# Performance work log

Hardware: AMD Instinct MI355X
Metric: run time of the kernel (lower is better)

## Reference

```python
import jax, jax.numpy as jnp
import numpy as np

EMBED_DIM = 1024
NUM_HEADS = 16
HEAD_DIM = EMBED_DIM // NUM_HEADS


def setup_inputs() -> dict:
    key = jax.random.key(0)
    ks = jax.random.split(key, 6)
    s = 1.0 / np.sqrt(EMBED_DIM)
    x = jax.random.normal(ks[0], (2, 2048, EMBED_DIM), dtype=jnp.float32)
    Wk = jax.random.uniform(ks[1], (EMBED_DIM, EMBED_DIM), jnp.float32, -s, s)
    Wq = jax.random.uniform(ks[2], (EMBED_DIM, EMBED_DIM), jnp.float32, -s, s)
    Wv = jax.random.uniform(ks[3], (EMBED_DIM, EMBED_DIM), jnp.float32, -s, s)
    Wo = jax.random.uniform(ks[4], (EMBED_DIM, EMBED_DIM), jnp.float32, -s, s)
    bo = jax.random.uniform(ks[5], (EMBED_DIM,), jnp.float32, -s, s)
    return {"x": x, "Wq": Wq, "Wk": Wk, "Wv": Wv, "Wo": Wo, "bo": bo}


def reference(x, Wq, Wk, Wv, Wo, bo):
    b, s, e = x.shape
    h, d = NUM_HEADS, HEAD_DIM
    scale = d ** (-0.5)
    # nn.Linear: y = x @ W.T ; here W stored as [out, in] -> use W.T
    q = (x @ Wq.T).reshape(b, s, h, d).transpose(0, 2, 1, 3)  # b h s d
    k = (x @ Wk.T).reshape(b, s, h, d).transpose(0, 2, 1, 3)
    v = (x @ Wv.T).reshape(b, s, h, d).transpose(0, 2, 1, 3)
    logits = jnp.einsum('bhqd,bhkd->bhqk', q, k) * scale
    attn = jax.nn.softmax(logits, axis=-1)
    out = jnp.einsum('bhqk,bhkd->bhqd', attn, v)
    out = out.transpose(0, 2, 1, 3).reshape(b, s, e)
    return out @ Wo.T + bo
```

## Files before the change

### kernel.cpp

```cpp
#include <hip/hip_runtime.h>
#include <hip/hip_bf16.h>

using short8 = __attribute__((ext_vector_type(8))) short;
using f32x4  = __attribute__((ext_vector_type(4))) float;
using uint4v = __attribute__((ext_vector_type(4))) unsigned;

#if __has_builtin(__builtin_amdgcn_exp2f)
#define EXP2(x) __builtin_amdgcn_exp2f(x)
#else
#define EXP2(x) exp2f(x)
#endif

#define SOFT_BARRIER()                                            \
    do {                                                          \
        asm volatile("s_waitcnt lgkmcnt(0)" ::: "memory");        \
        __builtin_amdgcn_s_barrier();                             \
    } while (0)

__device__ __forceinline__ short f2bf(float f) {
    union { float f; unsigned u; } v; v.f = f;
    unsigned r = v.u + 0x7fffu + ((v.u >> 16) & 1u);
    return (short)(r >> 16);
}
__device__ __forceinline__ unsigned pack_trunc(float a, float b) {
    union { float f; unsigned u; } ua, ub; ua.f = a; ub.f = b;
#if __has_builtin(__builtin_amdgcn_perm)
    return __builtin_amdgcn_perm(ub.u, ua.u, 0x07060302u);
#else
    return (ub.u & 0xFFFF0000u) | (ua.u >> 16);
#endif
}
__device__ __forceinline__ void async_copy16(const short* g, short* s) {
    __builtin_amdgcn_global_load_lds(
        (const __attribute__((address_space(1))) void*)g,
        (__attribute__((address_space(3))) void*)s, 16, 0, 0);
}

__global__ __launch_bounds__(256) void cvt_f32_bf16(
    const float* __restrict__ s0, const float* __restrict__ s1,
    const float* __restrict__ s2, const float* __restrict__ s3,
    const float* __restrict__ s4,
    short* __restrict__ d0, short* __restrict__ d1, short* __restrict__ d2,
    short* __restrict__ d3, short* __restrict__ d4) {
    const int bid = blockIdx.x;
    const float* s; short* d; int base;
    if (bid < 4096) {
        s = s0; d = d0; base = bid << 10;
    } else {
        const int r = bid - 4096;
        base = (r & 1023) << 10;
        switch (r >> 10) {
            case 0: s = s1; d = d1; break;
            case 1: s = s2; d = d2; break;
            case 2: s = s3; d = d3; break;
            default: s = s4; d = d4; break;
        }
    }
    const int idx = base + threadIdx.x * 4;
    float4 v = *(const float4*)(s + idx);
    short4 o;
    o.x = f2bf(v.x); o.y = f2bf(v.y); o.z = f2bf(v.z); o.w = f2bf(v.w);
    *(short4*)(d + idx) = o;
}

template <int MODE>
__device__ __forceinline__ void gemm_body(const short* __restrict__ A,
                                          const short* __restrict__ B,
                                          short* __restrict__ C,
                                          float scale,
                                          short* __restrict__ As,
                                          short* __restrict__ Bs,
                                          int bm, int bn) {
    constexpr int Kd = 1024, Nd = 1024, Sd = 2048;

    const int tid  = threadIdx.x;
    const int w    = tid >> 6, lane = tid & 63;
    const int quad = lane >> 4, l16 = lane & 15;
    const int xr   = l16 & 7;
    const int wm   = (w >> 1) * 64, wn = (w & 1) * 64;

    f32x4 acc[4][4];
#pragma unroll
    for (int i = 0; i < 4; ++i)
#pragma unroll
        for (int j = 0; j < 4; ++j) acc[i][j] = (f32x4){0.f, 0.f, 0.f, 0.f};

    for (int k0 = 0; k0 < Kd; k0 += 64) {
        __syncthreads();
#pragma unroll
        for (int c = 0; c < 4; ++c) {
            int li   = c * 256 + tid;
            int row  = li >> 3;
            int gcol = ((li & 7) ^ (row & 7)) * 8;
            async_copy16(A + (size_t)(bm + row) * Kd + k0 + gcol, &As[li * 8]);
            async_copy16(B + (size_t)(bn + row) * Kd + k0 + gcol, &Bs[li * 8]);
        }
        __syncthreads();

#pragma unroll
        for (int kk = 0; kk < 2; ++kk) {
            short8 af[4], bfv[4];
#pragma unroll
            for (int mi = 0; mi < 4; ++mi) {
                const int r = wm + mi * 16 + l16;
                af[mi] = *(const short8*)(
                    &As[r * 64 + (((kk * 4 + quad) ^ xr) * 8)]);
            }
#pragma unroll
            for (int ni = 0; ni < 4; ++ni) {
                const int r = wn + ni * 16 + l16;
                bfv[ni] = *(const short8*)(
                    &Bs[r * 64 + (((kk * 4 + quad) ^ xr) * 8)]);
            }
#pragma unroll
            for (int mi = 0; mi < 4; ++mi)
#pragma unroll
                for (int ni = 0; ni < 4; ++ni) {
                    if constexpr (MODE == 2)
                        acc[mi][ni] = __builtin_amdgcn_mfma_f32_16x16x32_bf16(
                            bfv[ni], af[mi], acc[mi][ni], 0, 0, 0);
                    else
                        acc[mi][ni] = __builtin_amdgcn_mfma_f32_16x16x32_bf16(
                            af[mi], bfv[ni], acc[mi][ni], 0, 0, 0);
                }
        }
    }

    if constexpr (MODE == 2) {
#pragma unroll
        for (int mi = 0; mi < 4; ++mi) {
            const int m_g = bm + wm + mi * 16 + l16;
            const int b_  = m_g >> 11, s_ = m_g & 2047;
#pragma unroll
            for (int ni = 0; ni < 4; ++ni)
#pragma unroll
                for (int r = 0; r < 4; ++r) {
                    const int n_g = bn + wn + ni * 16 + quad * 4 + r;
                    C[(size_t)b_ * Nd * Sd + (size_t)n_g * Sd + s_] =
                        f2bf(acc[mi][ni][r]);
                }
        }
    } else {
#pragma unroll
        for (int ni = 0; ni < 4; ++ni) {
            const int colg = bn + wn + ni * 16 + l16;
#pragma unroll
            for (int mi = 0; mi < 4; ++mi)
#pragma unroll
                for (int r = 0; r < 4; ++r) {
                    const int rowg = bm + wm + mi * 16 + quad * 4 + r;
                    C[(size_t)rowg * Nd + colg] = f2bf(acc[mi][ni][r] * scale);
                }
        }
    }
}

#define CSC 0.18033688f

__global__ __launch_bounds__(256, 3) void proj_gemm(
    const short* __restrict__ X,
    const short* __restrict__ Wq, const short* __restrict__ Wk,
    const short* __restrict__ Wv,
    short* __restrict__ Qo, short* __restrict__ Ko, short* __restrict__ VTo) {
    __shared__ __align__(16) short As[128 * 64];
    __shared__ __align__(16) short Bs[128 * 64];

    const int bid = blockIdx.x;
    const int xcd = bid & 7, idx = bid >> 3;
    const int z   = idx >> 5;
    const int rem = idx & 31;
    const int bm  = (((xcd >> 1) * 8) + (rem >> 2)) * 128;
    const int bn  = (((xcd & 1) * 4) + (rem & 3)) * 128;

    if (z == 0)
        gemm_body<0>(X, Wq, Qo, CSC, As, Bs, bm, bn);
    else if (z == 1)
        gemm_body<0>(X, Wk, Ko, 1.0f, As, Bs, bm, bn);
    else
        gemm_body<2>(X, Wv, VTo, 1.0f, As, Bs, bm, bn);
}

__global__ __launch_bounds__(256, 2) void out_gemm(
    const short* __restrict__ A, const short* __restrict__ B,
    const float* __restrict__ bias, float* __restrict__ C) {
    constexpr int Kd = 1024, Nd = 1024;
    __shared__ __align__(16) short As[64 * 64];
    __shared__ __align__(16) short Bs[128 * 64];

    const int tid  = threadIdx.x;
    const int w    = tid >> 6, lane = tid & 63;
    const int quad = lane >> 4, l16 = lane & 15;
    const int xr   = l16 & 7;
    const int wm   = (w >> 1) * 32, wn = (w & 1) * 64;

    const int bid = blockIdx.x;
    const int xcd = bid & 7, idx = bid >> 3;
    const int bm  = (((xcd >> 1) * 16) + (idx >> 2)) * 64;
    const int bn  = (((xcd & 1) * 4) + (idx & 3)) * 128;

    f32x4 acc[2][4];
#pragma unroll
    for (int i = 0; i < 2; ++i)
#pragma unroll
        for (int j = 0; j < 4; ++j) acc[i][j] = (f32x4){0.f, 0.f, 0.f, 0.f};

    for (int k0 = 0; k0 < Kd; k0 += 64) {
        __syncthreads();
#pragma unroll
        for (int c = 0; c < 2; ++c) {
            int li   = c * 256 + tid;
            int row  = li >> 3;
            int gcol = ((li & 7) ^ (row & 7)) * 8;
            async_copy16(A + (size_t)(bm + row) * Kd + k0 + gcol, &As[li * 8]);
        }
#pragma unroll
        for (int c = 0; c < 4; ++c) {
            int li   = c * 256 + tid;
            int row  = li >> 3;
            int gcol = ((li & 7) ^ (row & 7)) * 8;
            async_copy16(B + (size_t)(bn + row) * Kd + k0 + gcol, &Bs[li * 8]);
        }
        __syncthreads();

#pragma unroll
        for (int kk = 0; kk < 2; ++kk) {
            short8 af[2], bfv[4];
#pragma unroll
            for (int mi = 0; mi < 2; ++mi) {
                const int r = wm + mi * 16 + l16;
                af[mi] = *(const short8*)(
                    &As[r * 64 + (((kk * 4 + quad) ^ xr) * 8)]);
            }
#pragma unroll
            for (int ni = 0; ni < 4; ++ni) {
                const int r = wn + ni * 16 + l16;
                bfv[ni] = *(const short8*)(
                    &Bs[r * 64 + (((kk * 4 + quad) ^ xr) * 8)]);
            }
#pragma unroll
            for (int mi = 0; mi < 2; ++mi)
#pragma unroll
                for (int ni = 0; ni < 4; ++ni)
                    acc[mi][ni] = __builtin_amdgcn_mfma_f32_16x16x32_bf16(
                        af[mi], bfv[ni], acc[mi][ni], 0, 0, 0);
        }
    }

#pragma unroll
    for (int ni = 0; ni < 4; ++ni) {
        const int colg = bn + wn + ni * 16 + l16;
        const float bv = bias[colg];
#pragma unroll
        for (int mi = 0; mi < 2; ++mi)
#pragma unroll
            for (int r = 0; r < 4; ++r) {
                const int rowg = bm + wm + mi * 16 + quad * 4 + r;
                C[(size_t)rowg * Nd + colg] = acc[mi][ni][r] + bv;
            }
    }
}

__global__ __launch_bounds__(256, 2) void attn_kernel(
    const short* __restrict__ Q, const short* __restrict__ K,
    const short* __restrict__ VT, short* __restrict__ O) {
    constexpr int S = 2048, E = 1024, NT = S / 64;
    __shared__ __align__(16) short Ks[2][64 * 64];
    __shared__ __align__(16) short Vs[3][64 * 64];

    const int tid  = threadIdx.x;
    const int w    = tid >> 6, lane = tid & 63;
    const int quad = lane >> 4, l16 = lane & 15;

    const int bid  = blockIdx.x;
    const int xcd  = bid & 7, slot = bid >> 3;
    const int qt   = slot & 15;
    const int bh   = xcd + ((slot >> 4) << 3);
    const int b    = bh >> 4, h = bh & 15;

    const int    q0   = qt * 128 + w * 32;
    const size_t base = (size_t)b * S * E;
    const size_t vtb  = (size_t)b * E * S;
    const int    hc   = h * 64;
    const int    xr   = l16 & 7;

    short8 aq[2][2];
#pragma unroll
    for (int qg = 0; qg < 2; ++qg) {
        const short* qp = Q + base + (size_t)(q0 + qg * 16 + l16) * E + hc + quad * 8;
        aq[qg][0] = *(const short8*)(qp);
        aq[qg][1] = *(const short8*)(qp + 32);
    }

    f32x4 oT[2][4], o_sum[2];
#pragma unroll
    for (int qg = 0; qg < 2; ++qg) {
        o_sum[qg] = (f32x4){0.f, 0.f, 0.f, 0.f};
#pragma unroll
        for (int i = 0; i < 4; ++i) oT[qg][i] = (f32x4){0.f, 0.f, 0.f, 0.f};
    }

    int          kdst[2], vdst0[2], vdst1[2];
    const short* kga[2];
    const short* vga[2];
#pragma unroll
    for (int c = 0; c < 2; ++c) {
        int li = c * 256 + tid, row = li >> 3, cc = li & 7;
        kdst[c] = row * 64 + ((cc ^ (row & 7)) * 8);
        int c0   = 4 * (cc >> 2) + 2 * (cc & 1);
        int boff = 4 * ((cc >> 1) & 1);
        vdst0[c] = row * 64 + ((c0 ^ (row & 7)) * 8) + boff;
        vdst1[c] = row * 64 + (((c0 + 1) ^ (row & 7)) * 8) + boff;
        kga[c]   = K + base + (size_t)row * E + hc + cc * 8;
        vga[c]   = VT + vtb + (size_t)(hc + row) * S + cc * 8;
    }

    short8 kr[2], vr[2];
    auto load_regs = [&](int t) {
#pragma unroll
        for (int c = 0; c < 2; ++c) {
            kr[c] = *(const short8*)(kga[c] + (size_t)t * 64 * E);
            vr[c] = *(const short8*)(vga[c] + t * 64);
        }
    };
    auto store_regs = [&](short* Kn, short* Vn) {
#pragma unroll
        for (int c = 0; c < 2; ++c) {
            *(short8*)(&Kn[kdst[c]]) = kr[c];
            short4 lo, hi;
            lo.x = vr[c][0]; lo.y = vr[c][1]; lo.z = vr[c][2]; lo.w = vr[c][3];
            hi.x = vr[c][4]; hi.y = vr[c][5]; hi.z = vr[c][6]; hi.w = vr[c][7];
            *(short4*)(&Vn[vdst0[c]]) = lo;
            *(short4*)(&Vn[vdst1[c]]) = hi;
        }
    };

    const short8 ones = (short8){0x3F80, 0x3F80, 0x3F80, 0x3F80,
                                 0x3F80, 0x3F80, 0x3F80, 0x3F80};
    const float  LB   = 0.00281502f;

    uint4v pkvA[2][2], pkvB[2][2];

    auto qk_half = [&](const short* Kc, uint4v (&pc)[2][2], int h) {
#pragma unroll
        for (int kh = 0; kh < 2; ++kh) {
            const int    kn  = h * 2 + kh;
            const short* kb  = &Kc[(kn * 16 + l16) * 64];
            short8       bk0 = *(const short8*)(kb + ((quad ^ xr) * 8));
            short8       bk1 = *(const short8*)(kb + (((quad + 4) ^ xr) * 8));
#pragma unroll
            for (int qg = 0; qg < 2; ++qg) {
                f32x4 a = (f32x4){LB, LB, LB, LB};
                a = __builtin_amdgcn_mfma_f32_16x16x32_bf16(bk0, aq[qg][0], a, 0, 0, 0);
                a = __builtin_amdgcn_mfma_f32_16x16x32_bf16(bk1, aq[qg][1], a, 0, 0, 0);
                pc[qg][h][kh * 2]     = pack_trunc(EXP2(a[0]), EXP2(a[1]));
                pc[qg][h][kh * 2 + 1] = pack_trunc(EXP2(a[2]), EXP2(a[3]));
            }
        }
    };
    auto pv_half = [&](const short* Vp, uint4v (&pp)[2][2], int ks) {
        short8 pf[2];
#pragma unroll
        for (int qg = 0; qg < 2; ++qg) {
            union { uint4v u; short8 s; } cv;
            cv.u   = pp[qg][ks];
            pf[qg] = cv.s;
            o_sum[qg] = __builtin_amdgcn_mfma_f32_16x16x32_bf16(
                ones, pf[qg], o_sum[qg], 0, 0, 0);
        }
#pragma unroll
        for (int ni = 0; ni < 4; ++ni) {
            const int rv = ni * 16 + l16;
            short8 vb =
                *(const short8*)(&Vp[rv * 64 + (((ks * 4 + quad) ^ xr) * 8)]);
#pragma unroll
            for (int qg = 0; qg < 2; ++qg)
                oT[qg][ni] = __builtin_amdgcn_mfma_f32_16x16x32_bf16(
                    vb, pf[qg], oT[qg][ni], 0, 0, 0);
        }
    };

    auto body = [&](int kt, uint4v (&pp)[2][2], uint4v (&pc)[2][2]) {
        if (kt + 1 < NT) {
            store_regs(Ks[(kt + 1) & 1], Vs[(kt + 1) % 3]);
            if (kt + 2 < NT) load_regs(kt + 2);
        }
        const short* Kc = Ks[kt & 1];
        const short* Vp = Vs[(kt - 1) % 3];
        __builtin_amdgcn_s_setprio(1);
        pv_half(Vp, pp, 0);
        qk_half(Kc, pc, 0);
        pv_half(Vp, pp, 1);
        qk_half(Kc, pc, 1);
        __builtin_amdgcn_s_setprio(0);
        SOFT_BARRIER();
    };

    load_regs(0);
    store_regs(Ks[0], Vs[0]);
    load_regs(1);
    SOFT_BARRIER();
    store_regs(Ks[1], Vs[1]);
    load_regs(2);
    __builtin_amdgcn_s_setprio(1);
    qk_half(Ks[0], pkvA, 0);
    qk_half(Ks[0], pkvA, 1);
    __builtin_amdgcn_s_setprio(0);
    SOFT_BARRIER();

#pragma unroll 1
    for (int kt = 1; kt < NT - 1; kt += 2) {
        body(kt, pkvA, pkvB);
        body(kt + 1, pkvB, pkvA);
    }
    body(NT - 1, pkvA, pkvB);
    __builtin_amdgcn_s_setprio(1);
    pv_half(Vs[(NT - 1) % 3], pkvB, 0);
    pv_half(Vs[(NT - 1) % 3], pkvB, 1);
    __builtin_amdgcn_s_setprio(0);

#pragma unroll
    for (int qg = 0; qg < 2; ++qg) {
        const float inv = 1.0f / o_sum[qg][0];
        const int   qg_ = q0 + qg * 16 + l16;
#pragma unroll
        for (int ni = 0; ni < 4; ++ni) {
            short4 ov;
            ov.x = f2bf(oT[qg][ni][0] * inv);
            ov.y = f2bf(oT[qg][ni][1] * inv);
            ov.z = f2bf(oT[qg][ni][2] * inv);
            ov.w = f2bf(oT[qg][ni][3] * inv);
            *(short4*)(&O[base + (size_t)qg_ * E + hc + ni * 16 + quad * 4]) = ov;
        }
    }
}

extern "C" void kernel_launch(void* const* d_in, const int* in_sizes, int n_in,
                              void* d_out, int out_size, void* d_ws, size_t ws_size,
                              hipStream_t stream) {
    const float* x  = (const float*)d_in[0];
    const float* Wq = (const float*)d_in[1];
    const float* Wk = (const float*)d_in[2];
    const float* Wv = (const float*)d_in[3];
    const float* Wo = (const float*)d_in[4];
    const float* bo = (const float*)d_in[5];
    float* out = (float*)d_out;

    constexpr int XN = 2 * 2048 * 1024;
    constexpr int WN = 1024 * 1024;

    short* Xb  = (short*)d_ws;
    short* Wqb = Xb + XN;
    short* Wkb = Wqb + WN;
    short* Wvb = Wkb + WN;
    short* Wob = Wvb + WN;
    short* Qb  = Wob + WN;
    short* Kb  = Qb + XN;
    short* VTb = Kb + XN;

    cvt_f32_bf16<<<dim3(8192), 256, 0, stream>>>(
        x, Wq, Wk, Wv, Wo, Xb, Wqb, Wkb, Wvb, Wob);
    proj_gemm<<<dim3(768), 256, 0, stream>>>(Xb, Wqb, Wkb, Wvb, Qb, Kb, VTb);
    attn_kernel<<<dim3(512), 256, 0, stream>>>(Qb, Kb, VTb, Xb );
    out_gemm<<<dim3(512), 256, 0, stream>>>(Xb, Wob, bo, out);
}
```

Before: 162.9 us.

## Double-buffer LDS tiles in projection and output GEMMs to overlap loads with MFMA

Splits the shared-memory A/B tiles of both GEMM kernels into two buffers. While the current k-slice is computed, the async global-to-LDS copy for the next slice is issued, and each step uses a single vmcnt-wait barrier instead of two __syncthreads. This hides global load latency behind MFMA work. In exchange, LDS use per block doubles, so proj_gemm's launch bound drops from 3 to 2 blocks per CU, which may lower occupancy.

```diff
diff --git a/kernel.cpp b/kernel.cpp
--- a/kernel.cpp
+++ b/kernel.cpp
@@ -14,6 +14,12 @@
 #define SOFT_BARRIER()                                            \
     do {                                                          \
         asm volatile("s_waitcnt lgkmcnt(0)" ::: "memory");        \
+        __builtin_amdgcn_s_barrier();                             \
+    } while (0)
+
+#define VM_BARRIER()                                              \
+    do {                                                          \
+        asm volatile("s_waitcnt vmcnt(0)" ::: "memory");          \
         __builtin_amdgcn_s_barrier();                             \
     } while (0)
 
@@ -72,6 +78,7 @@
                                           short* __restrict__ Bs,
                                           int bm, int bn) {
     constexpr int Kd = 1024, Nd = 1024, Sd = 2048;
+    constexpr int BUF = 128 * 64;
 
     const int tid  = threadIdx.x;
     const int w    = tid >> 6, lane = tid & 63;
@@ -85,18 +92,26 @@
 #pragma unroll
         for (int j = 0; j < 4; ++j) acc[i][j] = (f32x4){0.f, 0.f, 0.f, 0.f};
 
-    for (int k0 = 0; k0 < Kd; k0 += 64) {
-        __syncthreads();
+    int lofs[4];
+    const short *aga[4], *bga[4];
+#pragma unroll
+    for (int c = 0; c < 4; ++c) {
+        const int li = c * 256 + tid, row = li >> 3;
+        const int gcol = ((li & 7) ^ (row & 7)) * 8;
+        lofs[c] = li * 8;
+        aga[c]  = A + (size_t)(bm + row) * Kd + gcol;
+        bga[c]  = B + (size_t)(bn + row) * Kd + gcol;
+    }
+
+    auto stage = [&](int k0, short* Ad, short* Bd) {
 #pragma unroll
         for (int c = 0; c < 4; ++c) {
-            int li   = c * 256 + tid;
-            int row  = li >> 3;
-            int gcol = ((li & 7) ^ (row & 7)) * 8;
-            async_copy16(A + (size_t)(bm + row) * Kd + k0 + gcol, &As[li * 8]);
-            async_copy16(B + (size_t)(bn + row) * Kd + k0 + gcol, &Bs[li * 8]);
-        }
-        __syncthreads();
-
+            async_copy16(aga[c] + k0, &Ad[lofs[c]]);
+            async_copy16(bga[c] + k0, &Bd[lofs[c]]);
+        }
+    };
+
+    auto compute = [&](const short* Ac, const short* Bc) {
 #pragma unroll
         for (int kk = 0; kk < 2; ++kk) {
             short8 af[4], bfv[4];
@@ -104,13 +119,13 @@
             for (int mi = 0; mi < 4; ++mi) {
                 const int r = wm + mi * 16 + l16;
                 af[mi] = *(const short8*)(
-                    &As[r * 64 + (((kk * 4 + quad) ^ xr) * 8)]);
+                    &Ac[r * 64 + (((kk * 4 + quad) ^ xr) * 8)]);
             }
 #pragma unroll
             for (int ni = 0; ni < 4; ++ni) {
                 const int r = wn + ni * 16 + l16;
                 bfv[ni] = *(const short8*)(
-                    &Bs[r * 64 + (((kk * 4 + quad) ^ xr) * 8)]);
+                    &Bc[r * 64 + (((kk * 4 + quad) ^ xr) * 8)]);
             }
 #pragma unroll
             for (int mi = 0; mi < 4; ++mi)
@@ -124,6 +139,18 @@
                             af[mi], bfv[ni], acc[mi][ni], 0, 0, 0);
                 }
         }
+    };
+
+    stage(0, As, Bs);
+    VM_BARRIER();
+
+#pragma unroll 1
+    for (int ks = 0; ks < 16; ++ks) {
+        if (ks + 1 < 16)
+            stage((ks + 1) * 64, As + ((ks + 1) & 1) * BUF,
+                  Bs + ((ks + 1) & 1) * BUF);
+        compute(As + (ks & 1) * BUF, Bs + (ks & 1) * BUF);
+        VM_BARRIER();
     }
 
     if constexpr (MODE == 2) {
@@ -157,13 +184,13 @@
 
 #define CSC 0.18033688f
 
-__global__ __launch_bounds__(256, 3) void proj_gemm(
+__global__ __launch_bounds__(256, 2) void proj_gemm(
     const short* __restrict__ X,
     const short* __restrict__ Wq, const short* __restrict__ Wk,
     const short* __restrict__ Wv,
     short* __restrict__ Qo, short* __restrict__ Ko, short* __restrict__ VTo) {
-    __shared__ __align__(16) short As[128 * 64];
-    __shared__ __align__(16) short Bs[128 * 64];
+    __shared__ __align__(16) short As[2 * 128 * 64];
+    __shared__ __align__(16) short Bs[2 * 128 * 64];
 
     const int bid = blockIdx.x;
     const int xcd = bid & 7, idx = bid >> 3;
@@ -184,8 +211,9 @@
     const short* __restrict__ A, const short* __restrict__ B,
     const float* __restrict__ bias, float* __restrict__ C) {
     constexpr int Kd = 1024, Nd = 1024;
-    __shared__ __align__(16) short As[64 * 64];
-    __shared__ __align__(16) short Bs[128 * 64];
+    constexpr int ABUF = 64 * 64, BBUF = 128 * 64;
+    __shared__ __align__(16) short As[2 * ABUF];
+    __shared__ __align__(16) short Bs[2 * BBUF];
 
     const int tid  = threadIdx.x;
     const int w    = tid >> 6, lane = tid & 63;
@@ -204,24 +232,31 @@
 #pragma unroll
         for (int j = 0; j < 4; ++j) acc[i][j] = (f32x4){0.f, 0.f, 0.f, 0.f};
 
-    for (int k0 = 0; k0 < Kd; k0 += 64) {
-        __syncthreads();
-#pragma unroll
-        for (int c = 0; c < 2; ++c) {
-            int li   = c * 256 + tid;
-            int row  = li >> 3;
-            int gcol = ((li & 7) ^ (row & 7)) * 8;
-            async_copy16(A + (size_t)(bm + row) * Kd + k0 + gcol, &As[li * 8]);
-        }
-#pragma unroll
-        for (int c = 0; c < 4; ++c) {
-            int li   = c * 256 + tid;
-            int row  = li >> 3;
-            int gcol = ((li & 7) ^ (row & 7)) * 8;
-            async_copy16(B + (size_t)(bn + row) * Kd + k0 + gcol, &Bs[li * 8]);
-        }
-        __syncthreads();
-
+    int aofs[2], bofs[4];
+    const short *aga[2], *bga[4];
+#pragma unroll
+    for (int c = 0; c < 2; ++c) {
+        const int li = c * 256 + tid, row = li >> 3;
+        const int gcol = ((li & 7) ^ (row & 7)) * 8;
+        aofs[c] = li * 8;
+        aga[c]  = A + (size_t)(bm + row) * Kd + gcol;
+    }
+#pragma unroll
+    for (int c = 0; c < 4; ++c) {
+        const int li = c * 256 + tid, row = li >> 3;
+        const int gcol = ((li & 7) ^ (row & 7)) * 8;
+        bofs[c] = li * 8;
+        bga[c]  = B + (size_t)(bn + row) * Kd + gcol;
+    }
+
+    auto stage = [&](int k0, short* Ad, short* Bd) {
+#pragma unroll
+        for (int c = 0; c < 2; ++c) async_copy16(aga[c] + k0, &Ad[aofs[c]]);
+#pragma unroll
+        for (int c = 0; c < 4; ++c) async_copy16(bga[c] + k0, &Bd[bofs[c]]);
+    };
+
+    auto compute = [&](const short* Ac, const short* Bc) {
 #pragma unroll
         for (int kk = 0; kk < 2; ++kk) {
             short8 af[2], bfv[4];
@@ -229,13 +264,13 @@
             for (int mi = 0; mi < 2; ++mi) {
                 const int r = wm + mi * 16 + l16;
                 af[mi] = *(const short8*)(
-                    &As[r * 64 + (((kk * 4 + quad) ^ xr) * 8)]);
+                    &Ac[r * 64 + (((kk * 4 + quad) ^ xr) * 8)]);
             }
 #pragma unroll
             for (int ni = 0; ni < 4; ++ni) {
                 const int r = wn + ni * 16 + l16;
                 bfv[ni] = *(const short8*)(
-                    &Bs[r * 64 + (((kk * 4 + quad) ^ xr) * 8)]);
+                    &Bc[r * 64 + (((kk * 4 + quad) ^ xr) * 8)]);
             }
 #pragma unroll
             for (int mi = 0; mi < 2; ++mi)
@@ -244,6 +279,18 @@
                     acc[mi][ni] = __builtin_amdgcn_mfma_f32_16x16x32_bf16(
                         af[mi], bfv[ni], acc[mi][ni], 0, 0, 0);
         }
+    };
+
+    stage(0, As, Bs);
+    VM_BARRIER();
+
+#pragma unroll 1
+    for (int ks = 0; ks < 16; ++ks) {
+        if (ks + 1 < 16)
+            stage((ks + 1) * 64, As + ((ks + 1) & 1) * ABUF,
+                  Bs + ((ks + 1) & 1) * BBUF);
+        compute(As + (ks & 1) * ABUF, Bs + (ks & 1) * BBUF);
+        VM_BARRIER();
     }
 
 #pragma unroll
```

Result: slower. 172.7 us (+6.1%).
